# Optimization experiments

Hardware: AMD Instinct MI355X
Metric: run time of the kernel (lower is better)

The kernel has to match this reference:

```python
import jax, jax.numpy as jnp
import numpy as np

EPS = 1e-5

def _ternary(w):
    # BitNet 1.58-bit: per-output-channel scale = median(|W|) (scale_op='median'),
    # quantize to {-1,0,1}*scale with straight-through estimator.
    s = jnp.maximum(jnp.median(jnp.abs(w), axis=(1, 2, 3), keepdims=True), EPS)
    q = jnp.clip(jnp.round(w / s), -1.0, 1.0) * s
    return w + jax.lax.stop_gradient(q - w)

def _conv3x3(x, w):
    # NCHW, OIHW, stride 1, pad 1 (spatial-preserving)
    return jax.lax.conv_general_dilated(
        x, _ternary(w), (1, 1), ((1, 1), (1, 1)),
        dimension_numbers=('NCHW', 'OIHW', 'NCHW'))

def _bn(y, g, b, m, v):
    # eval-mode BatchNorm2d folded to a single scale/shift
    inv = g / jnp.sqrt(v + EPS)
    return y * inv[None, :, None, None] + (b - m * inv)[None, :, None, None]

def _ssh(x, p):
    (w3, g3, b3, m3, v3,
     ws, gs, bs, ms, vs,
     w5, g5, b5, m5, v5,
     w7a, g7a, b7a, m7a, v7a,
     w7b, g7b, b7b, m7b, v7b) = p
    c3 = _bn(_conv3x3(x, w3), g3, b3, m3, v3)                      # [B, half, H, W]
    stem = jax.nn.silu(_bn(_conv3x3(x, ws), gs, bs, ms, vs))       # [B, quart, H, W]
    c5 = _bn(_conv3x3(stem, w5), g5, b5, m5, v5)                   # [B, quart, H, W]
    t = jax.nn.silu(_bn(_conv3x3(stem, w7a), g7a, b7a, m7a, v7a))
    c7 = _bn(_conv3x3(t, w7b), g7b, b7b, m7b, v7b)                 # [B, quart, H, W]
    return jax.nn.silu(jnp.concatenate((c3, c5, c7), axis=1))      # [B, out_ch, H, W]

def setup_inputs() -> dict:
    key = jax.random.key(0)
    B, CIN, H, W = 32, 256, 64, 64
    HALF, Q = 128, 64  # out_ch=256 -> half=128, quart=64
    d = {"x": jax.random.normal(jax.random.fold_in(key, 0), (B, CIN, H, W), jnp.float32)}

    def mk(i, o, c):
        k0, k1, k2, k3, k4 = jax.random.split(jax.random.fold_in(key, i), 5)
        return (jax.random.normal(k0, (o, c, 3, 3), jnp.float32) * 0.05,
                1.0 + 0.1 * jax.random.normal(k1, (o,), jnp.float32),   # gamma
                0.1 * jax.random.normal(k2, (o,), jnp.float32),          # beta
                0.1 * jax.random.normal(k3, (o,), jnp.float32),          # running mean
                0.5 + jax.random.uniform(k4, (o,), jnp.float32))         # running var > 0

    for name, (o, c), i in [("3", (HALF, CIN), 1), ("s", (Q, CIN), 2),
                            ("5", (Q, Q), 3), ("7a", (Q, Q), 4), ("7b", (Q, Q), 5)]:
        w, g, b, m, v = mk(i, o, c)
        d["w" + name] = w; d["g" + name] = g; d["b" + name] = b
        d["m" + name] = m; d["v" + name] = v
    return d

def reference(x,
              w3, g3, b3, m3, v3,
              ws, gs, bs, ms, vs,
              w5, g5, b5, m5, v5,
              w7a, g7a, b7a, m7a, v7a,
              w7b, g7b, b7b, m7b, v7b):
    return _ssh(x, (w3, g3, b3, m3, v3, ws, gs, bs, ms, vs,
                    w5, g5, b5, m5, v5, w7a, g7a, b7a, m7a, v7a,
                    w7b, g7b, b7b, m7b, v7b))
```

## Files before the change

kernel.cpp:

```cpp
#include <hip/hip_runtime.h>
#include <stdint.h>

#define EPSF 1e-5f

typedef __bf16 bf16;
typedef __attribute__((ext_vector_type(8))) __bf16 bf16x8;
typedef __attribute__((ext_vector_type(4))) float f32x4;

#define GL16(src, dst) __builtin_amdgcn_global_load_lds( \
    (const __attribute__((address_space(1))) void*)(src), \
    (__attribute__((address_space(3))) void*)(dst), 16, 0, 0)
#define MEMFENCE() asm volatile("" ::: "memory")

template<int N> __device__ __forceinline__ void vwait() {
  static_assert(N == 2 || N == 4 || N == 6, "unsupported vmcnt");
  if constexpr (N == 2) asm volatile("s_waitcnt vmcnt(2)" ::: "memory");
  else if constexpr (N == 4) asm volatile("s_waitcnt vmcnt(4)" ::: "memory");
  else asm volatile("s_waitcnt vmcnt(6)" ::: "memory");
}

struct QArgs {
  const float* w[5];
  const float* g[5];
  const float* bb[5];
  const float* m[5];
  const float* v[5];
  bf16* wpk[3];
  float* alpha[3];
  float* beta[3];
};

__global__ __launch_bounds__(256)
void quant_kernel(QArgs qa) {
  __shared__ int red[2][4];
  const int tid = threadIdx.x;
  const int blk = blockIdx.x;
  int layer, o;
  if (blk < 128)      { layer = 0; o = blk; }
  else if (blk < 192) { layer = 1; o = blk - 128; }
  else if (blk < 256) { layer = 2; o = blk - 192; }
  else if (blk < 320) { layer = 3; o = blk - 256; }
  else                { layer = 4; o = blk - 320; }
  const int I_[5]     = {256, 256, 64, 64, 64};
  const int gemm_[5]  = {0, 0, 1, 1, 2};
  const int obase_[5] = {0, 128, 0, 64, 0};
  const int gNMT[3]   = {12, 8, 4};
  const int I = I_[layer];
  const int n = I * 9;
  const float* w = qa.w[layer] + (size_t)o * n;

  unsigned key[9];
#pragma unroll
  for (int j = 0; j < 9; ++j) key[j] = 0xFFFFFFFFu;
  {
    int c2 = 0;
    for (int i = tid; i < n; i += 256) key[c2++] = __float_as_uint(fabsf(w[i]));
  }

  const int wv = tid >> 6;
  unsigned pfx[2] = {0u, 0u};
  const int rank0 = n / 2 - 1, rank1 = n / 2;
  int pp = 0;
  for (int bit = 31; bit >= 0; --bit) {
    const unsigned c0 = pfx[0] | (1u << bit);
    const unsigned c1 = pfx[1] | (1u << bit);
    int loc = 0;
#pragma unroll
    for (int j = 0; j < 9; ++j)
      loc += (key[j] < c0 ? 1 : 0) + (key[j] < c1 ? 0x10000 : 0);
    loc += __shfl_xor(loc, 32); loc += __shfl_xor(loc, 16);
    loc += __shfl_xor(loc, 8);  loc += __shfl_xor(loc, 4);
    loc += __shfl_xor(loc, 2);  loc += __shfl_xor(loc, 1);
    if ((tid & 63) == 0) red[pp][wv] = loc;
    __syncthreads();
    const int tot = red[pp][0] + red[pp][1] + red[pp][2] + red[pp][3];
    if ((tot & 0xFFFF) <= rank0) pfx[0] = c0;
    if ((tot >> 16)    <= rank1) pfx[1] = c1;
    pp ^= 1;
  }
  const float s =
      fmaxf(0.5f * (__uint_as_float(pfx[0]) + __uint_as_float(pfx[1])), EPSF);

  const int g  = gemm_[layer];
  const int ob = obase_[layer];
  const int NMT = gNMT[g];
  if (tid == 0) {
    float inv = qa.g[layer][o] / sqrtf(qa.v[layer][o] + EPSF);
    qa.alpha[g][ob + o] = s * inv;
    qa.beta[g][ob + o]  = qa.bb[layer][o] - qa.m[layer][o] * inv;
  }
  const int og  = ob + o;
  const int mt  = og >> 4;
  const int l16 = og & 15;
  bf16* wp = qa.wpk[g];
  for (int i = tid; i < n; i += 256) {
    float t = rintf(w[i] / s);
    t = fmaxf(-1.f, fminf(1.f, t));
    int c = i / 9, pos = i % 9;
    int k = pos * I + c;
    int ks = k >> 5, kq = (k >> 3) & 3, jj = k & 7;
    wp[((size_t)((ks * NMT + mt) * 64 + kq * 16 + l16)) * 8 + jj] = (bf16)t;
  }
}

__global__ __launch_bounds__(256)
void transpose_k(const float* __restrict__ x, bf16* __restrict__ xT,
                 float* __restrict__ zp) {
  if (blockIdx.x == 0 && threadIdx.x < 32) zp[threadIdx.x] = 0.0f;
  __shared__ float tile[64 * 66];
  const int tid = threadIdx.x;
  const int blk = blockIdx.x;
  const int cg = blk & 3;
  const int h  = (blk >> 2) & 63;
  const int b  = blk >> 8;
  const int w4 = (tid & 15) * 4;
  const int cb = tid >> 4;
#pragma unroll
  for (int p = 0; p < 4; ++p) {
    int c = cb + p * 16;
    const float4 v =
        *(const float4*)&x[(((size_t)(b * 256 + cg * 64 + c)) * 64 + h) * 64 + w4];
    tile[(w4 + 0) * 66 + c] = v.x;
    tile[(w4 + 1) * 66 + c] = v.y;
    tile[(w4 + 2) * 66 + c] = v.z;
    tile[(w4 + 3) * 66 + c] = v.w;
  }
  __syncthreads();
#pragma unroll
  for (int p = 0; p < 2; ++p) {
    int id = tid + p * 256;
    int c8 = id & 7, w2 = id >> 3;
    const float* src = &tile[w2 * 66 + c8 * 8];
    float2 f0 = *(const float2*)(src + 0);
    float2 f1 = *(const float2*)(src + 2);
    float2 f2 = *(const float2*)(src + 4);
    float2 f3 = *(const float2*)(src + 6);
    bf16x8 v;
    v[0] = (bf16)f0.x; v[1] = (bf16)f0.y; v[2] = (bf16)f1.x; v[3] = (bf16)f1.y;
    v[4] = (bf16)f2.x; v[5] = (bf16)f2.y; v[6] = (bf16)f3.x; v[7] = (bf16)f3.y;
    *(bf16x8*)&xT[(((size_t)(b * 64 + h)) * 64 + w2) * 256 + cg * 64 + c8 * 8] = v;
  }
}

template<int CIN, int NMT, int MM, int C1, bool HASPAD, int TPB, int RB, bool XSWZ>
__global__ __launch_bounds__(TPB, 4)
void conv_k(const bf16* __restrict__ xin,
            const bf16* __restrict__ wpk,
            const float* __restrict__ alpha,
            const float* __restrict__ beta,
            float* __restrict__ out, int chan_off,
            bf16* __restrict__ padout,
            const bf16* __restrict__ zpage) {
  constexpr int NC    = CIN / 32;
  constexpr int NG    = NMT / MM;
  constexpr int RS    = RB + 2;
  constexpr int NCHK  = RS * 66 * 4;
  constexpr int SLOTS = (RB == 2) ? 1088 : 1600;
  constexpr int BUFB  = SLOTS * 16;
  constexpr int P     = (NCHK + TPB - 1) / TPB;
  constexpr int HT    = 64 / RB;
  constexpr int NBLK  = 32 * HT;

  __shared__ __align__(16) union U {
    bf16 xs[2][SLOTS * 8];
    bf16 ep[RB * 64 * 72];
  } sm;

  const int tid  = threadIdx.x;
  const int wave = tid >> 6;
  const int lane = tid & 63;
  const int q    = lane >> 4;
  const int t16  = lane & 15;
  const int rw   = wave / NG;
  const int mt0  = (wave % NG) * MM;
  const int wg   = (int)blockIdx.x;
  const int wgid = XSWZ ? (wg & 7) * (NBLK / 8) + (wg >> 3) : wg;
  const int b    = wgid / HT;
  const int h0   = (wgid % HT) * RB;

  const bf16* srcp[P];
  int step[P];
#pragma unroll
  for (int p = 0; p < P; ++p) {
    const int id = tid + p * TPB;
    const int c8p = id & 3, rj = id >> 2;
    const int j = rj % 66, r = rj / 66;
    const int hh = h0 + r - 1, ww = j - 1;
    const bool v = (id < NCHK) && ((unsigned)hh < 64u) && ((unsigned)ww < 64u);
    const int c8 = c8p ^ ((j >> 1) & 3);
    srcp[p] = v ? &xin[(((size_t)(b * 64 + hh)) * 64 + ww) * CIN + c8 * 8] : zpage;
    step[p] = v ? 32 : 0;
  }

  auto stage = [&](char* base, bool second) {
#pragma unroll
    for (int p = 0; p < P; ++p) {
      if ((p + 1) * TPB <= NCHK || p * TPB + wave * 64 < NCHK)
        GL16(srcp[p] + (second ? step[p] : 0), base + (p * TPB + wave * 64) * 16);
    }
  };

  int Caddr[3];
#pragma unroll
  for (int kw = 0; kw < 3; ++kw) {
    const int col = t16 + kw;
    Caddr[kw] = rw * 4224 + col * 64 + ((q ^ ((col >> 1) & 3)) << 4);
  }

  char* const lds0 = (char*)&sm.xs[0][0];

  stage(lds0, false);
  if constexpr (NC == 2) {
    stage(lds0 + BUFB, true);
  } else {
#pragma unroll
    for (int p = 0; p < P; ++p) srcp[p] += step[p];
  }
  MEMFENCE();

  bf16x8 fr[3][MM];
#pragma unroll
  for (int mm = 0; mm < MM; ++mm) {
    fr[0][mm] = *(const bf16x8*)&wpk[((size_t)(mt0 + mm) * 64 + lane) * 8];
    fr[1][mm] = *(const bf16x8*)&wpk[((size_t)(NC * NMT + mt0 + mm) * 64 + lane) * 8];
  }

  f32x4 acc[4][MM] = {};
  int tog = BUFB;

  for (int ci = 0; ci < NC; ++ci) {
    if (NC > 2 || ci == 0) {
      vwait<2 * MM>();
      __builtin_amdgcn_s_barrier();
    }
    if constexpr (NC > 2) {
      if (ci + 1 < NC) {
        stage(lds0 + (((ci + 1) & 1) ? BUFB : 0), false);
#pragma unroll
        for (int p = 0; p < P; ++p) srcp[p] += step[p];
      }
    }
    MEMFENCE();
    __builtin_amdgcn_s_setprio(1);
#pragma unroll
    for (int pos = 0; pos < 9; ++pos) {
      const int t = pos + 2;
      if (t <= 8) {
        const int ksn = t * NC + ci;
#pragma unroll
        for (int mm = 0; mm < MM; ++mm)
          fr[t % 3][mm] = *(const bf16x8*)&wpk[((size_t)(ksn * NMT + mt0 + mm) * 64 + lane) * 8];
      } else if (ci + 1 < NC) {
        const int ksn = (t - 9) * NC + (ci + 1);
#pragma unroll
        for (int mm = 0; mm < MM; ++mm)
          fr[t % 3][mm] = *(const bf16x8*)&wpk[((size_t)(ksn * NMT + mt0 + mm) * 64 + lane) * 8];
      }
      const int kh = pos / 3, kw = pos % 3;
#pragma unroll
      for (int nt = 0; nt < 4; ++nt) {
        const bf16x8 bv =
            *(const bf16x8*)(lds0 + (Caddr[kw] + nt * 1024 + kh * 4224));
#pragma unroll
        for (int mm = 0; mm < MM; ++mm)
          acc[nt][mm] = __builtin_amdgcn_mfma_f32_16x16x32_bf16(fr[pos % 3][mm], bv, acc[nt][mm], 0, 0, 0);
      }
    }
    __builtin_amdgcn_s_setprio(0);
#pragma unroll
    for (int kw = 0; kw < 3; ++kw) Caddr[kw] += tog;
    tog = -tog;
  }

  const int h = h0 + rw;
#pragma unroll
  for (int mm = 0; mm < MM; ++mm) {
    const int o0 = (mt0 + mm) * 16 + 4 * q;
    float av[4], bv2[4];
#pragma unroll
    for (int i = 0; i < 4; ++i) { av[i] = alpha[o0 + i]; bv2[i] = beta[o0 + i]; }
#pragma unroll
    for (int nt = 0; nt < 4; ++nt) {
      const int wv = nt * 16 + t16;
#pragma unroll
      for (int i = 0; i < 4; ++i) {
        float v = acc[nt][mm][i] * av[i] + bv2[i];
        float sg = v / (1.f + __expf(-v));
        acc[nt][mm][i] = sg;
        if (o0 < C1)
          out[(((size_t)(b * 256 + chan_off + o0 + i)) * 64 + h) * 64 + wv] = sg;
      }
    }
  }
  if (HASPAD) {
    __syncthreads();
#pragma unroll
    for (int mm = 0; mm < MM; ++mm) {
      const int o0 = (mt0 + mm) * 16 + 4 * q;
      if (o0 >= C1) {
#pragma unroll
        for (int nt = 0; nt < 4; ++nt) {
          const int px = rw * 64 + nt * 16 + t16;
          union { bf16 h4[4]; uint2 u; } pk;
#pragma unroll
          for (int i = 0; i < 4; ++i) pk.h4[i] = (bf16)acc[nt][mm][i];
          *(uint2*)&sm.ep[px * 72 + (o0 - C1)] = pk.u;
        }
      }
    }
    __syncthreads();
    constexpr int EPP = (RB * 64 * 8) / TPB;
#pragma unroll
    for (int p = 0; p < EPP; ++p) {
      int id = tid + p * TPB;
      int c8 = id & 7, px = id >> 3;
      bf16x8 v = *(const bf16x8*)&sm.ep[px * 72 + c8 * 8];
      const int r = px >> 6, wv2 = px & 63;
      *(bf16x8*)&padout[(((size_t)(b * 64 + h0 + r)) * 64 + wv2) * 64 + c8 * 8] = v;
    }
  }
}

extern "C" void kernel_launch(void* const* d_in, const int* in_sizes, int n_in,
                              void* d_out, int out_size, void* d_ws, size_t ws_size,
                              hipStream_t stream) {
  QArgs qa;
  const float* x = (const float*)d_in[0];
  for (int L = 0; L < 5; ++L) {
    qa.w[L]  = (const float*)d_in[1 + 5 * L];
    qa.g[L]  = (const float*)d_in[2 + 5 * L];
    qa.bb[L] = (const float*)d_in[3 + 5 * L];
    qa.m[L]  = (const float*)d_in[4 + 5 * L];
    qa.v[L]  = (const float*)d_in[5 + 5 * L];
  }
  char* p = (char*)d_ws;
  bf16* wpk1 = (bf16*)p; p += (size_t)192 * 2304 * 2;
  bf16* wpk2 = (bf16*)p; p += (size_t)128 * 576 * 2;
  bf16* wpk3 = (bf16*)p; p += (size_t)64 * 576 * 2;
  float* a1 = (float*)p; p += 1024;
  float* b1 = (float*)p; p += 1024;
  float* a2 = (float*)p; p += 1024;
  float* b2 = (float*)p; p += 1024;
  float* a3 = (float*)p; p += 1024;
  float* b3 = (float*)p; p += 1024;
  float* zp = (float*)p; p += 128;
  bf16* xT   = (bf16*)p; p += (size_t)32 * 64 * 64 * 256 * 2;
  bf16* stem = (bf16*)p; p += (size_t)32 * 64 * 64 * 64 * 2;
  bf16* tbuf = xT;
  qa.wpk[0] = wpk1; qa.wpk[1] = wpk2; qa.wpk[2] = wpk3;
  qa.alpha[0] = a1; qa.alpha[1] = a2; qa.alpha[2] = a3;
  qa.beta[0]  = b1; qa.beta[1]  = b2; qa.beta[2]  = b3;

  quant_kernel<<<384, 256, 0, stream>>>(qa);
  transpose_k<<<32 * 64 * 4, 256, 0, stream>>>(x, xT, zp);

  const bf16* zpb = (const bf16*)zp;
  conv_k<256, 12, 3, 128, true,  512, 2, false><<<1024,  512, 0, stream>>>(xT,   wpk1, a1, b1, (float*)d_out, 0,   stem, zpb);
  conv_k< 64,  8, 2,  64, true, 1024, 4, true ><<< 512, 1024, 0, stream>>>(stem, wpk2, a2, b2, (float*)d_out, 128, tbuf, zpb);
  conv_k< 64,  4, 2,  64, false, 512, 4, true ><<< 512,  512, 0, stream>>>(tbuf, wpk3, a3, b3, (float*)d_out, 192, nullptr, zpb);
}
```

Measured before the change: 435.2 us.

## Merge quant and transpose kernels; double-buffer LDS B-fragments and weight fragments in conv

Merges the weight-quantization and input-transpose kernels into one launch, with block ranges dispatching to each role, which removes a launch and lets both phases run concurrently. In the conv inner loop, the 3-deep weight-fragment ring becomes an even/odd double buffer. LDS B-fragments for the next tap are prefetched into registers before the current tap's MFMAs run, and the initial vmcnt wait is adjusted to match. This is meant to hide LDS read latency behind the MFMAs, at the cost of more VGPRs and a shorter prefetch distance for the global weight loads.

```diff
diff --git a/kernel.cpp b/kernel.cpp
--- a/kernel.cpp
+++ b/kernel.cpp
@@ -13,8 +13,9 @@
 #define MEMFENCE() asm volatile("" ::: "memory")
 
 template<int N> __device__ __forceinline__ void vwait() {
-  static_assert(N == 2 || N == 4 || N == 6, "unsupported vmcnt");
+  static_assert(N == 2 || N == 3 || N == 4 || N == 6, "unsupported vmcnt");
   if constexpr (N == 2) asm volatile("s_waitcnt vmcnt(2)" ::: "memory");
+  else if constexpr (N == 3) asm volatile("s_waitcnt vmcnt(3)" ::: "memory");
   else if constexpr (N == 4) asm volatile("s_waitcnt vmcnt(4)" ::: "memory");
   else asm volatile("s_waitcnt vmcnt(6)" ::: "memory");
 }
@@ -31,85 +32,85 @@
 };
 
 __global__ __launch_bounds__(256)
-void quant_kernel(QArgs qa) {
+void prep_k(QArgs qa, const float* __restrict__ x, bf16* __restrict__ xT,
+            float* __restrict__ zp) {
   __shared__ int red[2][4];
-  const int tid = threadIdx.x;
-  const int blk = blockIdx.x;
-  int layer, o;
-  if (blk < 128)      { layer = 0; o = blk; }
-  else if (blk < 192) { layer = 1; o = blk - 128; }
-  else if (blk < 256) { layer = 2; o = blk - 192; }
-  else if (blk < 320) { layer = 3; o = blk - 256; }
-  else                { layer = 4; o = blk - 320; }
-  const int I_[5]     = {256, 256, 64, 64, 64};
-  const int gemm_[5]  = {0, 0, 1, 1, 2};
-  const int obase_[5] = {0, 128, 0, 64, 0};
-  const int gNMT[3]   = {12, 8, 4};
-  const int I = I_[layer];
-  const int n = I * 9;
-  const float* w = qa.w[layer] + (size_t)o * n;
-
-  unsigned key[9];
-#pragma unroll
-  for (int j = 0; j < 9; ++j) key[j] = 0xFFFFFFFFu;
-  {
-    int c2 = 0;
-    for (int i = tid; i < n; i += 256) key[c2++] = __float_as_uint(fabsf(w[i]));
-  }
-
-  const int wv = tid >> 6;
-  unsigned pfx[2] = {0u, 0u};
-  const int rank0 = n / 2 - 1, rank1 = n / 2;
-  int pp = 0;
-  for (int bit = 31; bit >= 0; --bit) {
-    const unsigned c0 = pfx[0] | (1u << bit);
-    const unsigned c1 = pfx[1] | (1u << bit);
-    int loc = 0;
-#pragma unroll
-    for (int j = 0; j < 9; ++j)
-      loc += (key[j] < c0 ? 1 : 0) + (key[j] < c1 ? 0x10000 : 0);
-    loc += __shfl_xor(loc, 32); loc += __shfl_xor(loc, 16);
-    loc += __shfl_xor(loc, 8);  loc += __shfl_xor(loc, 4);
-    loc += __shfl_xor(loc, 2);  loc += __shfl_xor(loc, 1);
-    if ((tid & 63) == 0) red[pp][wv] = loc;
-    __syncthreads();
-    const int tot = red[pp][0] + red[pp][1] + red[pp][2] + red[pp][3];
-    if ((tot & 0xFFFF) <= rank0) pfx[0] = c0;
-    if ((tot >> 16)    <= rank1) pfx[1] = c1;
-    pp ^= 1;
-  }
-  const float s =
-      fmaxf(0.5f * (__uint_as_float(pfx[0]) + __uint_as_float(pfx[1])), EPSF);
-
-  const int g  = gemm_[layer];
-  const int ob = obase_[layer];
-  const int NMT = gNMT[g];
-  if (tid == 0) {
-    float inv = qa.g[layer][o] / sqrtf(qa.v[layer][o] + EPSF);
-    qa.alpha[g][ob + o] = s * inv;
-    qa.beta[g][ob + o]  = qa.bb[layer][o] - qa.m[layer][o] * inv;
-  }
-  const int og  = ob + o;
-  const int mt  = og >> 4;
-  const int l16 = og & 15;
-  bf16* wp = qa.wpk[g];
-  for (int i = tid; i < n; i += 256) {
-    float t = rintf(w[i] / s);
-    t = fmaxf(-1.f, fminf(1.f, t));
-    int c = i / 9, pos = i % 9;
-    int k = pos * I + c;
-    int ks = k >> 5, kq = (k >> 3) & 3, jj = k & 7;
-    wp[((size_t)((ks * NMT + mt) * 64 + kq * 16 + l16)) * 8 + jj] = (bf16)t;
-  }
-}
-
-__global__ __launch_bounds__(256)
-void transpose_k(const float* __restrict__ x, bf16* __restrict__ xT,
-                 float* __restrict__ zp) {
-  if (blockIdx.x == 0 && threadIdx.x < 32) zp[threadIdx.x] = 0.0f;
   __shared__ float tile[64 * 66];
   const int tid = threadIdx.x;
-  const int blk = blockIdx.x;
+  if (blockIdx.x == 0 && tid < 32) zp[tid] = 0.0f;
+
+  if (blockIdx.x < 384) {
+    const int blk = blockIdx.x;
+    int layer, o;
+    if (blk < 128)      { layer = 0; o = blk; }
+    else if (blk < 192) { layer = 1; o = blk - 128; }
+    else if (blk < 256) { layer = 2; o = blk - 192; }
+    else if (blk < 320) { layer = 3; o = blk - 256; }
+    else                { layer = 4; o = blk - 320; }
+    const int I_[5]     = {256, 256, 64, 64, 64};
+    const int gemm_[5]  = {0, 0, 1, 1, 2};
+    const int obase_[5] = {0, 128, 0, 64, 0};
+    const int gNMT[3]   = {12, 8, 4};
+    const int I = I_[layer];
+    const int n = I * 9;
+    const float* w = qa.w[layer] + (size_t)o * n;
+
+    unsigned key[9];
+#pragma unroll
+    for (int j = 0; j < 9; ++j) key[j] = 0xFFFFFFFFu;
+    {
+      int c2 = 0;
+      for (int i = tid; i < n; i += 256) key[c2++] = __float_as_uint(fabsf(w[i]));
+    }
+
+    const int wv = tid >> 6;
+    unsigned pfx[2] = {0u, 0u};
+    const int rank0 = n / 2 - 1, rank1 = n / 2;
+    int pp = 0;
+    for (int bit = 31; bit >= 0; --bit) {
+      const unsigned c0 = pfx[0] | (1u << bit);
+      const unsigned c1 = pfx[1] | (1u << bit);
+      int loc = 0;
+#pragma unroll
+      for (int j = 0; j < 9; ++j)
+        loc += (key[j] < c0 ? 1 : 0) + (key[j] < c1 ? 0x10000 : 0);
+      loc += __shfl_xor(loc, 32); loc += __shfl_xor(loc, 16);
+      loc += __shfl_xor(loc, 8);  loc += __shfl_xor(loc, 4);
+      loc += __shfl_xor(loc, 2);  loc += __shfl_xor(loc, 1);
+      if ((tid & 63) == 0) red[pp][wv] = loc;
+      __syncthreads();
+      const int tot = red[pp][0] + red[pp][1] + red[pp][2] + red[pp][3];
+      if ((tot & 0xFFFF) <= rank0) pfx[0] = c0;
+      if ((tot >> 16)    <= rank1) pfx[1] = c1;
+      pp ^= 1;
+    }
+    const float s =
+        fmaxf(0.5f * (__uint_as_float(pfx[0]) + __uint_as_float(pfx[1])), EPSF);
+
+    const int g  = gemm_[layer];
+    const int ob = obase_[layer];
+    const int NMT = gNMT[g];
+    if (tid == 0) {
+      float inv = qa.g[layer][o] / sqrtf(qa.v[layer][o] + EPSF);
+      qa.alpha[g][ob + o] = s * inv;
+      qa.beta[g][ob + o]  = qa.bb[layer][o] - qa.m[layer][o] * inv;
+    }
+    const int og  = ob + o;
+    const int mt  = og >> 4;
+    const int l16 = og & 15;
+    bf16* wp = qa.wpk[g];
+    for (int i = tid; i < n; i += 256) {
+      float t = rintf(w[i] / s);
+      t = fmaxf(-1.f, fminf(1.f, t));
+      int c = i / 9, pos = i % 9;
+      int k = pos * I + c;
+      int ks = k >> 5, kq = (k >> 3) & 3, jj = k & 7;
+      wp[((size_t)((ks * NMT + mt) * 64 + kq * 16 + l16)) * 8 + jj] = (bf16)t;
+    }
+    return;
+  }
+
+  const int blk = blockIdx.x - 384;
   const int cg = blk & 3;
   const int h  = (blk >> 2) & 63;
   const int b  = blk >> 8;
@@ -218,18 +219,19 @@
   }
   MEMFENCE();
 
-  bf16x8 fr[3][MM];
-#pragma unroll
-  for (int mm = 0; mm < MM; ++mm) {
-    fr[0][mm] = *(const bf16x8*)&wpk[((size_t)(mt0 + mm) * 64 + lane) * 8];
-    fr[1][mm] = *(const bf16x8*)&wpk[((size_t)(NC * NMT + mt0 + mm) * 64 + lane) * 8];
-  }
+  bf16x8 aE[MM], aO[MM];
+#pragma unroll
+  for (int mm = 0; mm < MM; ++mm)
+    aE[mm] = *(const bf16x8*)&wpk[((size_t)(mt0 + mm) * 64 + lane) * 8];
 
   f32x4 acc[4][MM] = {};
   int tog = BUFB;
 
   for (int ci = 0; ci < NC; ++ci) {
-    if (NC > 2 || ci == 0) {
+    if (ci == 0) {
+      vwait<MM>();
+      __builtin_amdgcn_s_barrier();
+    } else if constexpr (NC > 2) {
       vwait<2 * MM>();
       __builtin_amdgcn_s_barrier();
     }
@@ -241,29 +243,38 @@
       }
     }
     MEMFENCE();
+    bf16x8 bb0[4], bb1[4];
+#pragma unroll
+    for (int nt = 0; nt < 4; ++nt)
+      bb0[nt] = *(const bf16x8*)(lds0 + (Caddr[0] + nt * 1024));
     __builtin_amdgcn_s_setprio(1);
 #pragma unroll
     for (int pos = 0; pos < 9; ++pos) {
-      const int t = pos + 2;
-      if (t <= 8) {
-        const int ksn = t * NC + ci;
+      bf16x8* bc = (pos & 1) ? bb1 : bb0;
+      bf16x8* bn = (pos & 1) ? bb0 : bb1;
+      if (pos < 8) {
+        const int kh1 = (pos + 1) / 3, kw1 = (pos + 1) % 3;
+#pragma unroll
+        for (int nt = 0; nt < 4; ++nt)
+          bn[nt] = *(const bf16x8*)(lds0 + (Caddr[kw1] + nt * 1024 + kh1 * 4224));
+      }
+      bf16x8* ac = (pos & 1) ? aO : aE;
+      bf16x8* an = (pos & 1) ? aE : aO;
+      if (pos < 8) {
+        const int ksn = (pos + 1) * NC + ci;
 #pragma unroll
         for (int mm = 0; mm < MM; ++mm)
-          fr[t % 3][mm] = *(const bf16x8*)&wpk[((size_t)(ksn * NMT + mt0 + mm) * 64 + lane) * 8];
-      } else if (ci + 1 < NC) {
-        const int ksn = (t - 9) * NC + (ci + 1);
+          an[mm] = *(const bf16x8*)&wpk[((size_t)(ksn * NMT + mt0 + mm) * 64 + lane) * 8];
+      }
+#pragma unroll
+      for (int nt = 0; nt < 4; ++nt)
 #pragma unroll
         for (int mm = 0; mm < MM; ++mm)
-          fr[t % 3][mm] = *(const bf16x8*)&wpk[((size_t)(ksn * NMT + mt0 + mm) * 64 + lane) * 8];
-      }
-      const int kh = pos / 3, kw = pos % 3;
-#pragma unroll
-      for (int nt = 0; nt < 4; ++nt) {
-        const bf16x8 bv =
-            *(const bf16x8*)(lds0 + (Caddr[kw] + nt * 1024 + kh * 4224));
+          acc[nt][mm] = __builtin_amdgcn_mfma_f32_16x16x32_bf16(ac[mm], bc[nt], acc[nt][mm], 0, 0, 0);
+      if (pos == 8 && ci + 1 < NC) {
 #pragma unroll
         for (int mm = 0; mm < MM; ++mm)
-          acc[nt][mm] = __builtin_amdgcn_mfma_f32_16x16x32_bf16(fr[pos % 3][mm], bv, acc[nt][mm], 0, 0, 0);
+          aE[mm] = *(const bf16x8*)&wpk[((size_t)((ci + 1) * NMT + mt0 + mm) * 64 + lane) * 8];
       }
     }
     __builtin_amdgcn_s_setprio(0);
@@ -351,8 +362,7 @@
   qa.alpha[0] = a1; qa.alpha[1] = a2; qa.alpha[2] = a3;
   qa.beta[0]  = b1; qa.beta[1]  = b2; qa.beta[2]  = b3;
 
-  quant_kernel<<<384, 256, 0, stream>>>(qa);
-  transpose_k<<<32 * 64 * 4, 256, 0, stream>>>(x, xT, zp);
+  prep_k<<<384 + 32 * 64 * 4, 256, 0, stream>>>(qa, x, xT, zp);
 
   const bf16* zpb = (const bf16*)zp;
   conv_k<256, 12, 3, 128, true,  512, 2, false><<<1024,  512, 0, stream>>>(xT,   wpk1, a1, b1, (float*)d_out, 0,   stem, zpb);
```

Result: faster. 415.8 us (median of 2 runs) (-4.4%).
